# Optimization experiments

Measured on AMD Instinct MI355X. Metric: run time of the kernel, lower is better.

Reference implementation:

```python
import jax, jax.numpy as jnp
import numpy as np

N_NODES = 100000
N_EDGES = 1600000
DIM = 128


def setup_inputs() -> dict:
    key = jax.random.key(0)
    k1, k2, k3, k4 = jax.random.split(key, 4)
    x = jax.random.normal(k1, (N_NODES, DIM), dtype=jnp.float32)
    edge_index = jax.random.randint(k2, (2, N_EDGES), 0, N_NODES, dtype=jnp.int64)
    scale = 1.0 / np.sqrt(DIM)
    W1 = jax.random.normal(k3, (DIM, DIM), dtype=jnp.float32) * scale
    W2 = jax.random.normal(k4, (DIM, DIM), dtype=jnp.float32) * scale
    b1 = jnp.zeros((DIM,), dtype=jnp.float32)
    b2 = jnp.zeros((DIM,), dtype=jnp.float32)
    return {"x": x, "edge_index": edge_index, "W1": W1, "b1": b1, "W2": W2, "b2": b2}


def _gcn_conv(x, src, dst, dinv, W, b, n):
    # linear transform first (PyG GCNConv), then normalized scatter-add aggregation
    h = x @ W                                   # [N, out]
    norm = dinv[src] * dinv[dst]                # [E+N]
    msg = h[src] * norm[:, None]                # [E+N, out]
    agg = jax.ops.segment_sum(msg, dst, num_segments=n)
    return agg + b


def reference(x, edge_index, W1, b1, W2, b2):
    n = x.shape[0]
    loops = jnp.arange(n, dtype=edge_index.dtype)
    src = jnp.concatenate([edge_index[0], loops])  # add self-loops
    dst = jnp.concatenate([edge_index[1], loops])
    deg = jax.ops.segment_sum(jnp.ones_like(src, dtype=x.dtype), dst, num_segments=n)
    dinv = jnp.where(deg > 0, jax.lax.rsqrt(deg), 0.0)  # D^{-1/2}
    h = _gcn_conv(x, src, dst, dinv, W1, b1, n)
    h = jax.nn.relu(h)
    out = _gcn_conv(h, src, dst, dinv, W2, b2, n)
    return out
```

## Files before the change

### kernel.cpp

```cpp
#include <hip/hip_runtime.h>
#include <hip/hip_bf16.h>
#include <hip/hip_fp16.h>

#define NN 100000
#define DIM 128
#define NB 391
#define BCAP 5120
#define SCAN_NB 391
#define GTILES ((NN + 63) / 64)

__global__ void k_zero(int* __restrict__ p, int n) {
    int i = blockIdx.x * blockDim.x + threadIdx.x;
    if (i < n) p[i] = 0;
}

__global__ void k_binA(const int* __restrict__ src, const int* __restrict__ dst,
                       int* __restrict__ bcur, int* __restrict__ binbuf, int E) {
    __shared__ int hist[NB];
    __shared__ int base[NB];
    const int t = threadIdx.x;
    for (int b = t; b < NB; b += 256) hist[b] = 0;
    __syncthreads();

    const int e0 = blockIdx.x * 4096;
    int mys[16], myd[16];
#pragma unroll
    for (int i = 0; i < 16; ++i) {
        const int e = e0 + i * 256 + t;
        int d = -1, s = 0;
        if (e < E) {
            d = dst[e];
            s = src[e];
            atomicAdd(&hist[d >> 8], 1);
        }
        mys[i] = s;
        myd[i] = d;
    }
    __syncthreads();

    for (int b = t; b < NB; b += 256) {
        const int h = hist[b];
        base[b] = h ? atomicAdd(&bcur[b], h) : 0;
    }
    __syncthreads();
    for (int b = t; b < NB; b += 256) hist[b] = 0;
    __syncthreads();

#pragma unroll
    for (int i = 0; i < 16; ++i) {
        const int d = myd[i];
        if (d >= 0) {
            const int b = d >> 8;
            const int loc = atomicAdd(&hist[b], 1);
            const int p = base[b] + loc;
            if (p < BCAP) binbuf[b * BCAP + p] = mys[i] | ((d & 255) << 17);
        }
    }
}

__global__ void k_binCount(const int* __restrict__ bcur, const int* __restrict__ binbuf,
                           int* __restrict__ degi) {
    __shared__ int cnt[256];
    const int b = blockIdx.x;
    const int t = threadIdx.x;
    cnt[t] = 0;
    __syncthreads();
    const int n = min(bcur[b], BCAP);
    const int* p = &binbuf[b * BCAP];
    for (int i = t; i < n; i += 256) atomicAdd(&cnt[p[i] >> 17], 1);
    __syncthreads();
    const int node = b * 256 + t;
    if (node < NN) degi[node] = cnt[t];
}

__global__ void k_scan1(const int* __restrict__ deg, int* __restrict__ bsum, int n) {
    __shared__ int red[256];
    const int t = threadIdx.x;
    const int i = blockIdx.x * 256 + t;
    red[t] = (i < n) ? deg[i] : 0;
    __syncthreads();
    for (int d = 128; d > 0; d >>= 1) {
        if (t < d) red[t] += red[t + d];
        __syncthreads();
    }
    if (t == 0) bsum[blockIdx.x] = red[0];
}

__global__ void k_scan2(int* __restrict__ bsum, int nb) {
    __shared__ int s[1024];
    const int t = threadIdx.x;
    const int v = (t < nb) ? bsum[t] : 0;
    s[t] = v;
    __syncthreads();
    int acc = v;
    for (int d = 1; d < 1024; d <<= 1) {
        const int o = (t >= d) ? s[t - d] : 0;
        __syncthreads();
        acc += o;
        s[t] = acc;
        __syncthreads();
    }
    if (t < nb) bsum[t] = acc - v;
}

__global__ void k_scan3d(const int* __restrict__ deg, const int* __restrict__ bsum,
                         int* __restrict__ rowptr, float* __restrict__ dinv, int n) {
    __shared__ int s[256];
    const int t = threadIdx.x;
    const int i = blockIdx.x * 256 + t;
    const int v = (i < n) ? deg[i] : 0;
    s[t] = v;
    __syncthreads();
    int acc = v;
    for (int d = 1; d < 256; d <<= 1) {
        const int o = (t >= d) ? s[t - d] : 0;
        __syncthreads();
        acc += o;
        s[t] = acc;
        __syncthreads();
    }
    const int ex = acc - v + bsum[blockIdx.x];
    if (i < n) {
        rowptr[i] = ex;
        dinv[i] = rsqrtf((float)(v + 1));
        if (i == n - 1) rowptr[n] = ex + v;
    }
}

template <int IN_HALF, int FILL>
__global__ void k_gemm(const float* __restrict__ inF, const __half* __restrict__ inH,
                       const float* __restrict__ W, const float* __restrict__ dinv,
                       const float* __restrict__ bin, __half* __restrict__ outH,
                       const int* __restrict__ rowptr, const int* __restrict__ bcur,
                       const int* __restrict__ binbuf, int* __restrict__ csr) {
    __shared__ float wt[32][DIM];
    __shared__ float xt[64][32];
    __shared__ int cur[256];
    const int t = threadIdx.x;

    if (FILL && blockIdx.x < NB) {
        const int b = blockIdx.x;
        const int node = b * 256 + t;
        cur[t] = (node < NN) ? rowptr[node] : 0;
        __syncthreads();
        const int n = min(bcur[b], BCAP);
        const int* p = &binbuf[b * BCAP];
        for (int i = t; i < n; i += 256) {
            const int v = p[i];
            const int pos = atomicAdd(&cur[v >> 17], 1);
            csr[pos] = v & 0x1FFFF;
        }
        return;
    }

    const int tile = blockIdx.x - (FILL ? NB : 0);
    const int row0 = tile * 64;
    const int g  = t >> 5;
    const int r0 = g << 3;
    const int c4 = (t & 31) << 2;

    float4 acc[8] = {};

    for (int kt = 0; kt < DIM; kt += 32) {
#pragma unroll
        for (int j = 0; j < 4; ++j) {
            const int i = t + j * 256;
            const int kr = i >> 5;
            const int kc = (i & 31) << 2;
            *(float4*)&wt[kr][kc] = *(const float4*)&W[(kt + kr) * DIM + kc];
        }
#pragma unroll
        for (int j = 0; j < 2; ++j) {
            const int i = t + j * 256;
            const int r = i >> 3;
            const int kc = (i & 7) << 2;
            const int row = row0 + r;
            float4 v = {0.f, 0.f, 0.f, 0.f};
            if constexpr (IN_HALF) {
                if (row < NN) {
                    const __half2 h0 = *(const __half2*)&inH[row * DIM + kt + kc];
                    const __half2 h1 = *(const __half2*)&inH[row * DIM + kt + kc + 2];
                    const float2 f0 = __half22float2(h0);
                    const float2 f1 = __half22float2(h1);
                    const float dr = dinv[row];
                    const float4 bb = *(const float4*)&bin[kt + kc];
                    v.x = fmaxf(fmaf(dr, f0.x, bb.x), 0.f);
                    v.y = fmaxf(fmaf(dr, f0.y, bb.y), 0.f);
                    v.z = fmaxf(fmaf(dr, f1.x, bb.z), 0.f);
                    v.w = fmaxf(fmaf(dr, f1.y, bb.w), 0.f);
                }
            } else {
                if (row < NN) v = *(const float4*)&inF[row * DIM + kt + kc];
            }
            *(float4*)&xt[r][kc] = v;
        }
        __syncthreads();

#pragma unroll
        for (int kk = 0; kk < 32; kk += 4) {
            const float4 w0 = *(const float4*)&wt[kk][c4];
            const float4 w1 = *(const float4*)&wt[kk + 1][c4];
            const float4 w2 = *(const float4*)&wt[kk + 2][c4];
            const float4 w3 = *(const float4*)&wt[kk + 3][c4];
#pragma unroll
            for (int i = 0; i < 8; ++i) {
                const float4 xv = *(const float4*)&xt[r0 + i][kk];
                acc[i].x = fmaf(xv.x, w0.x, fmaf(xv.y, w1.x, fmaf(xv.z, w2.x, fmaf(xv.w, w3.x, acc[i].x))));
                acc[i].y = fmaf(xv.x, w0.y, fmaf(xv.y, w1.y, fmaf(xv.z, w2.y, fmaf(xv.w, w3.y, acc[i].y))));
                acc[i].z = fmaf(xv.x, w0.z, fmaf(xv.y, w1.z, fmaf(xv.z, w2.z, fmaf(xv.w, w3.z, acc[i].z))));
                acc[i].w = fmaf(xv.x, w0.w, fmaf(xv.y, w1.w, fmaf(xv.z, w2.w, fmaf(xv.w, w3.w, acc[i].w))));
            }
        }
        __syncthreads();
    }

#pragma unroll
    for (int i = 0; i < 8; ++i) {
        const int row = row0 + r0 + i;
        if (row < NN) {
            const float d = dinv[row];
            union { __half2 h2[2]; uint2 u; } pk;
            pk.h2[0] = __floats2half2_rn(acc[i].x * d, acc[i].y * d);
            pk.h2[1] = __floats2half2_rn(acc[i].z * d, acc[i].w * d);
            *(uint2*)&outH[row * DIM + c4] = pk.u;
        }
    }
}

template <int FINAL>
__global__ void k_gather(const __half* __restrict__ hs, __half* __restrict__ outH,
                         float* __restrict__ outF, const int* __restrict__ csr,
                         const int* __restrict__ rowptr, const float* __restrict__ dinv,
                         const float* __restrict__ b2) {
    const int w = (blockIdx.x * blockDim.x + threadIdx.x) >> 6;
    if (w >= NN) return;
    const int lane = threadIdx.x & 63;
    const int off  = lane << 1;

    const int start = __builtin_amdgcn_readfirstlane(rowptr[w]);
    const int end   = __builtin_amdgcn_readfirstlane(rowptr[w + 1]);

    float2 a0 = __half22float2(*(const __half2*)&hs[w * DIM + off]);
    float2 a1 = {0.f, 0.f}, a2 = {0.f, 0.f}, a3 = {0.f, 0.f};

    int j = start;
    for (; j + 3 < end; j += 4) {
        const int s0 = __builtin_amdgcn_readfirstlane(csr[j]);
        const int s1 = __builtin_amdgcn_readfirstlane(csr[j + 1]);
        const int s2 = __builtin_amdgcn_readfirstlane(csr[j + 2]);
        const int s3 = __builtin_amdgcn_readfirstlane(csr[j + 3]);
        const float2 v0 = __half22float2(*(const __half2*)&hs[s0 * DIM + off]);
        const float2 v1 = __half22float2(*(const __half2*)&hs[s1 * DIM + off]);
        const float2 v2 = __half22float2(*(const __half2*)&hs[s2 * DIM + off]);
        const float2 v3 = __half22float2(*(const __half2*)&hs[s3 * DIM + off]);
        a0.x += v0.x; a0.y += v0.y;
        a1.x += v1.x; a1.y += v1.y;
        a2.x += v2.x; a2.y += v2.y;
        a3.x += v3.x; a3.y += v3.y;
    }
    for (; j < end; ++j) {
        const int s0 = __builtin_amdgcn_readfirstlane(csr[j]);
        const float2 v0 = __half22float2(*(const __half2*)&hs[s0 * DIM + off]);
        a0.x += v0.x; a0.y += v0.y;
    }

    float2 r = {a0.x + a1.x + a2.x + a3.x, a0.y + a1.y + a2.y + a3.y};
    if constexpr (FINAL) {
        const float d = dinv[w];
        const float2 b = *(const float2*)&b2[off];
        r.x = fmaf(d, r.x, b.x);
        r.y = fmaf(d, r.y, b.y);
        *(float2*)&outF[w * DIM + off] = r;
    } else {
        *(__half2*)&outH[w * DIM + off] = __floats2half2_rn(r.x, r.y);
    }
}

extern "C" void kernel_launch(void* const* d_in, const int* in_sizes, int n_in,
                              void* d_out, int out_size, void* d_ws, size_t ws_size,
                              hipStream_t stream) {
    const float* x  = (const float*)d_in[0];
    const int*   ei = (const int*)d_in[1];
    const float* W1 = (const float*)d_in[2];
    const float* b1 = (const float*)d_in[3];
    const float* W2 = (const float*)d_in[4];
    const float* b2 = (const float*)d_in[5];
    float* out = (float*)d_out;

    const int E = in_sizes[1] / 2;
    const int* src = ei;
    const int* dst = ei + E;

    char* ws = (char*)d_ws;
    float*  dinv   = (float*)(ws);
    int*    degi   = (int*)  (ws + (1  << 20));
    int*    rowptr = (int*)  (ws + (2  << 20));
    int*    bsum   = (int*)  (ws + (3  << 20));
    int*    bcur   = (int*)  (ws + (3  << 20) + 65536);
    int*    csr    = (int*)  (ws + (4  << 20));
    int*    binbuf = (int*)  (ws + (11 << 20));
    __half* hs     = (__half*)(ws + (20 << 20));
    __half* agg1   = (__half*)(ws + (47 << 20));

    const int ABLK = (E + 4095) / 4096;

    k_zero    <<<(NB + 255) / 256, 256, 0, stream>>>(bcur, NB);
    k_binA    <<<ABLK, 256, 0, stream>>>(src, dst, bcur, binbuf, E);
    k_binCount<<<NB, 256, 0, stream>>>(bcur, binbuf, degi);
    k_scan1   <<<SCAN_NB, 256, 0, stream>>>(degi, bsum, NN);
    k_scan2   <<<1, 1024, 0, stream>>>(bsum, SCAN_NB);
    k_scan3d  <<<SCAN_NB, 256, 0, stream>>>(degi, bsum, rowptr, dinv, NN);

    k_gemm<0, 1><<<NB + GTILES, 256, 0, stream>>>(x, nullptr, W1, dinv, nullptr, hs,
                                                  rowptr, bcur, binbuf, csr);
    k_gather<0> <<<(NN * 64) / 256, 256, 0, stream>>>(hs, agg1, nullptr, csr, rowptr,
                                                      dinv, nullptr);

    k_gemm<1, 0><<<GTILES, 256, 0, stream>>>(nullptr, agg1, W2, dinv, b1, hs,
                                             rowptr, bcur, binbuf, csr);
    k_gather<1> <<<(NN * 64) / 256, 256, 0, stream>>>(hs, nullptr, out, csr, rowptr,
                                                      dinv, b2);
}
```

Measured before the change: 269.8 us.

## Replace FP32 shared-memory GEMM with register-resident f16 MFMA matrix-core GEMM

Rewrites the dense transform kernel to use the 16x16x32 f16 MFMA instruction instead of scalar FMA over LDS tiles. Each wave keeps its W column slice in registers as f16 fragments and loads activation fragments straight from global memory, converting them to f16. This removes LDS staging and barriers and moves the work onto matrix cores. In exchange, inputs and weights are rounded to f16 before multiplying, W is fetched with strided scalar loads per block, and the output is written with narrower scattered stores.

```diff
diff --git a/kernel.cpp b/kernel.cpp
--- a/kernel.cpp
+++ b/kernel.cpp
@@ -8,6 +8,9 @@
 #define BCAP 5120
 #define SCAN_NB 391
 #define GTILES ((NN + 63) / 64)
+
+typedef _Float16 f16x8 __attribute__((ext_vector_type(8)));
+typedef float f32x4 __attribute__((ext_vector_type(4)));
 
 __global__ void k_zero(int* __restrict__ p, int n) {
     int i = blockIdx.x * blockDim.x + threadIdx.x;
@@ -128,13 +131,11 @@
 }
 
 template <int IN_HALF, int FILL>
-__global__ void k_gemm(const float* __restrict__ inF, const __half* __restrict__ inH,
+__global__ void k_gemm(const float* __restrict__ inF, const _Float16* __restrict__ inH,
                        const float* __restrict__ W, const float* __restrict__ dinv,
-                       const float* __restrict__ bin, __half* __restrict__ outH,
+                       const float* __restrict__ bin, _Float16* __restrict__ outH,
                        const int* __restrict__ rowptr, const int* __restrict__ bcur,
                        const int* __restrict__ binbuf, int* __restrict__ csr) {
-    __shared__ float wt[32][DIM];
-    __shared__ float xt[64][32];
     __shared__ int cur[256];
     const int t = threadIdx.x;
 
@@ -155,74 +156,84 @@
 
     const int tile = blockIdx.x - (FILL ? NB : 0);
     const int row0 = tile * 64;
-    const int g  = t >> 5;
-    const int r0 = g << 3;
-    const int c4 = (t & 31) << 2;
-
-    float4 acc[8] = {};
-
-    for (int kt = 0; kt < DIM; kt += 32) {
-#pragma unroll
-        for (int j = 0; j < 4; ++j) {
-            const int i = t + j * 256;
-            const int kr = i >> 5;
-            const int kc = (i & 31) << 2;
-            *(float4*)&wt[kr][kc] = *(const float4*)&W[(kt + kr) * DIM + kc];
-        }
-#pragma unroll
-        for (int j = 0; j < 2; ++j) {
-            const int i = t + j * 256;
-            const int r = i >> 3;
-            const int kc = (i & 7) << 2;
-            const int row = row0 + r;
-            float4 v = {0.f, 0.f, 0.f, 0.f};
+    const int wv   = t >> 6;
+    const int l    = t & 63;
+    const int l15  = l & 15;
+    const int lk8  = (l >> 4) << 3;
+    const int colw = wv << 5;
+
+    f16x8 bf[2][4];
+#pragma unroll
+    for (int ct = 0; ct < 2; ++ct) {
+#pragma unroll
+        for (int kt = 0; kt < 4; ++kt) {
+            const int n  = colw + ct * 16 + l15;
+            const int k0 = kt * 32 + lk8;
+            f16x8 v;
+#pragma unroll
+            for (int j = 0; j < 8; ++j) v[j] = (_Float16)W[(k0 + j) * DIM + n];
+            bf[ct][kt] = v;
+        }
+    }
+
+    f32x4 acc[4][2];
+#pragma unroll
+    for (int rt = 0; rt < 4; ++rt)
+#pragma unroll
+        for (int ct = 0; ct < 2; ++ct) acc[rt][ct] = (f32x4){0.f, 0.f, 0.f, 0.f};
+
+#pragma unroll
+    for (int rt = 0; rt < 4; ++rt) {
+        int row = row0 + rt * 16 + l15;
+        row = min(row, NN - 1);
+        f16x8 a[4];
+#pragma unroll
+        for (int kt = 0; kt < 4; ++kt) {
+            const int k0 = kt * 32 + lk8;
             if constexpr (IN_HALF) {
-                if (row < NN) {
-                    const __half2 h0 = *(const __half2*)&inH[row * DIM + kt + kc];
-                    const __half2 h1 = *(const __half2*)&inH[row * DIM + kt + kc + 2];
-                    const float2 f0 = __half22float2(h0);
-                    const float2 f1 = __half22float2(h1);
-                    const float dr = dinv[row];
-                    const float4 bb = *(const float4*)&bin[kt + kc];
-                    v.x = fmaxf(fmaf(dr, f0.x, bb.x), 0.f);
-                    v.y = fmaxf(fmaf(dr, f0.y, bb.y), 0.f);
-                    v.z = fmaxf(fmaf(dr, f1.x, bb.z), 0.f);
-                    v.w = fmaxf(fmaf(dr, f1.y, bb.w), 0.f);
-                }
+                const f16x8 h = *(const f16x8*)&inH[row * DIM + k0];
+                const float dr = dinv[row];
+                const float4 bb0 = *(const float4*)&bin[k0];
+                const float4 bb1 = *(const float4*)&bin[k0 + 4];
+                f16x8 v;
+                v[0] = (_Float16)fmaxf(fmaf(dr, (float)h[0], bb0.x), 0.f);
+                v[1] = (_Float16)fmaxf(fmaf(dr, (float)h[1], bb0.y), 0.f);
+                v[2] = (_Float16)fmaxf(fmaf(dr, (float)h[2], bb0.z), 0.f);
+                v[3] = (_Float16)fmaxf(fmaf(dr, (float)h[3], bb0.w), 0.f);
+                v[4] = (_Float16)fmaxf(fmaf(dr, (float)h[4], bb1.x), 0.f);
+                v[5] = (_Float16)fmaxf(fmaf(dr, (float)h[5], bb1.y), 0.f);
+                v[6] = (_Float16)fmaxf(fmaf(dr, (float)h[6], bb1.z), 0.f);
+                v[7] = (_Float16)fmaxf(fmaf(dr, (float)h[7], bb1.w), 0.f);
+                a[kt] = v;
             } else {
-                if (row < NN) v = *(const float4*)&inF[row * DIM + kt + kc];
+                const float4 v0 = *(const float4*)&inF[row * DIM + k0];
+                const float4 v1 = *(const float4*)&inF[row * DIM + k0 + 4];
+                f16x8 v;
+                v[0] = (_Float16)v0.x; v[1] = (_Float16)v0.y;
+                v[2] = (_Float16)v0.z; v[3] = (_Float16)v0.w;
+                v[4] = (_Float16)v1.x; v[5] = (_Float16)v1.y;
+                v[6] = (_Float16)v1.z; v[7] = (_Float16)v1.w;
+                a[kt] = v;
             }
-            *(float4*)&xt[r][kc] = v;
-        }
-        __syncthreads();
-
-#pragma unroll
-        for (int kk = 0; kk < 32; kk += 4) {
-            const float4 w0 = *(const float4*)&wt[kk][c4];
-            const float4 w1 = *(const float4*)&wt[kk + 1][c4];
-            const float4 w2 = *(const float4*)&wt[kk + 2][c4];
-            const float4 w3 = *(const float4*)&wt[kk + 3][c4];
-#pragma unroll
-            for (int i = 0; i < 8; ++i) {
-                const float4 xv = *(const float4*)&xt[r0 + i][kk];
-                acc[i].x = fmaf(xv.x, w0.x, fmaf(xv.y, w1.x, fmaf(xv.z, w2.x, fmaf(xv.w, w3.x, acc[i].x))));
-                acc[i].y = fmaf(xv.x, w0.y, fmaf(xv.y, w1.y, fmaf(xv.z, w2.y, fmaf(xv.w, w3.y, acc[i].y))));
-                acc[i].z = fmaf(xv.x, w0.z, fmaf(xv.y, w1.z, fmaf(xv.z, w2.z, fmaf(xv.w, w3.z, acc[i].z))));
-                acc[i].w = fmaf(xv.x, w0.w, fmaf(xv.y, w1.w, fmaf(xv.z, w2.w, fmaf(xv.w, w3.w, acc[i].w))));
+        }
+#pragma unroll
+        for (int ct = 0; ct < 2; ++ct)
+#pragma unroll
+            for (int kt = 0; kt < 4; ++kt)
+                acc[rt][ct] = __builtin_amdgcn_mfma_f32_16x16x32_f16(a[kt], bf[ct][kt],
+                                                                    acc[rt][ct], 0, 0, 0);
+    }
+
+#pragma unroll
+    for (int rt = 0; rt < 4; ++rt) {
+#pragma unroll
+        for (int r = 0; r < 4; ++r) {
+            const int row = row0 + rt * 16 + ((l >> 4) << 2) + r;
+            if (row < NN) {
+                const float d = dinv[row];
+                outH[row * DIM + colw + l15]      = (_Float16)(acc[rt][0][r] * d);
+                outH[row * DIM + colw + 16 + l15] = (_Float16)(acc[rt][1][r] * d);
             }
-        }
-        __syncthreads();
-    }
-
-#pragma unroll
-    for (int i = 0; i < 8; ++i) {
-        const int row = row0 + r0 + i;
-        if (row < NN) {
-            const float d = dinv[row];
-            union { __half2 h2[2]; uint2 u; } pk;
-            pk.h2[0] = __floats2half2_rn(acc[i].x * d, acc[i].y * d);
-            pk.h2[1] = __floats2half2_rn(acc[i].z * d, acc[i].w * d);
-            *(uint2*)&outH[row * DIM + c4] = pk.u;
         }
     }
 }
@@ -292,15 +303,15 @@
     const int* dst = ei + E;
 
     char* ws = (char*)d_ws;
-    float*  dinv   = (float*)(ws);
-    int*    degi   = (int*)  (ws + (1  << 20));
-    int*    rowptr = (int*)  (ws + (2  << 20));
-    int*    bsum   = (int*)  (ws + (3  << 20));
-    int*    bcur   = (int*)  (ws + (3  << 20) + 65536);
-    int*    csr    = (int*)  (ws + (4  << 20));
-    int*    binbuf = (int*)  (ws + (11 << 20));
-    __half* hs     = (__half*)(ws + (20 << 20));
-    __half* agg1   = (__half*)(ws + (47 << 20));
+    float*    dinv   = (float*)(ws);
+    int*      degi   = (int*)  (ws + (1  << 20));
+    int*      rowptr = (int*)  (ws + (2  << 20));
+    int*      bsum   = (int*)  (ws + (3  << 20));
+    int*      bcur   = (int*)  (ws + (3  << 20) + 65536);
+    int*      csr    = (int*)  (ws + (4  << 20));
+    int*      binbuf = (int*)  (ws + (11 << 20));
+    _Float16* hs     = (_Float16*)(ws + (20 << 20));
+    _Float16* agg1   = (_Float16*)(ws + (47 << 20));
 
     const int ABLK = (E + 4095) / 4096;
 
@@ -313,11 +324,11 @@
 
     k_gemm<0, 1><<<NB + GTILES, 256, 0, stream>>>(x, nullptr, W1, dinv, nullptr, hs,
                                                   rowptr, bcur, binbuf, csr);
-    k_gather<0> <<<(NN * 64) / 256, 256, 0, stream>>>(hs, agg1, nullptr, csr, rowptr,
-                                                      dinv, nullptr);
+    k_gather<0> <<<(NN * 64) / 256, 256, 0, stream>>>((const __half*)hs, (__half*)agg1,
+                                                      nullptr, csr, rowptr, dinv, nullptr);
 
     k_gemm<1, 0><<<GTILES, 256, 0, stream>>>(nullptr, agg1, W2, dinv, b1, hs,
                                              rowptr, bcur, binbuf, csr);
-    k_gather<1> <<<(NN * 64) / 256, 256, 0, stream>>>(hs, nullptr, out, csr, rowptr,
-                                                      dinv, b2);
-}
+    k_gather<1> <<<(NN * 64) / 256, 256, 0, stream>>>((const __half*)hs, nullptr, out,
+                                                      csr, rowptr, dinv, b2);
+}
```

Result: faster. 236.7 us (-12.3%).
